# Optimization experiments

Measured on AMD Instinct MI355X. Metric: run time of the kernel, lower is better.

## Reference

```python
import jax, jax.numpy as jnp
import numpy as np

N = 4096      # nodes
INS = 256     # input feature dim
OUTS = 64     # per-mechanism output dim
M = 4         # N_mechs
LEAK = 0.2    # leaky relu negative slope
NEG_INF = -1e9


def setup_inputs() -> dict:
    key = jax.random.key(0)
    ks = jax.random.split(key, 7)
    x = jax.random.normal(ks[0], (N, INS), dtype=jnp.float32)
    adj = jax.random.randint(ks[1], (N, N), 0, 2).astype(jnp.int32)
    W = jax.random.normal(ks[2], (M, INS, OUTS), dtype=jnp.float32) * 0.1
    a1 = jax.random.normal(ks[3], (M, OUTS), dtype=jnp.float32) * 0.1
    a2 = jax.random.normal(ks[4], (M, OUTS), dtype=jnp.float32) * 0.1
    Wc = jax.random.normal(ks[5], (INS, 2 * M * OUTS), dtype=jnp.float32) * 0.1
    bc = jnp.zeros((2 * M * OUTS,), dtype=jnp.float32)
    return {"x": x, "adj": adj, "W": W, "a1": a1, "a2": a2, "Wc": Wc, "bc": bc}


def reference(x, adj, W, a1, a2, Wc, bc):
    # conditioner: mean-pool nodes -> linear -> (gamma, beta) per mechanism
    pooled = x.mean(axis=0)                                   # [INS]
    gb = (pooled @ Wc + bc).reshape(2, M, OUTS)
    gamma, beta = gb[0], gb[1]                                # [M, OUTS] each

    # per-mechanism linear transform + FiLM modulation
    h = jnp.einsum('ni,mio->mno', x, W)                       # [M, N, OUTS]
    h = gamma[:, None, :] * h + beta[:, None, :]

    # GAT-style decomposed attention logits: e_ij = leaky_relu(a1.h_i + a2.h_j)
    e_src = jnp.einsum('mno,mo->mn', h, a1)                   # [M, N]
    e_dst = jnp.einsum('mno,mo->mn', h, a2)                   # [M, N]
    e = e_src[:, :, None] + e_dst[:, None, :]                 # [M, N, N]
    e = jnp.where(e > 0, e, LEAK * e)                         # leaky relu

    # mask by adjacency, softmax over neighbors
    e = jnp.where(adj[None] > 0, e, jnp.float32(NEG_INF))
    attn = jax.nn.softmax(e, axis=-1)                         # [M, N, N]

    out = jnp.einsum('mnk,mko->mno', attn, h)                 # [M, N, OUTS]
    out = jnp.transpose(out, (1, 0, 2)).reshape(N, M * OUTS)  # concat dim=1
    return jax.nn.elu(out)                                    # activate=True
```

## Files before the change

### kernel.cpp

```cpp
#include <hip/hip_runtime.h>
#include <hip/hip_bf16.h>

#define NN    4096
#define INS_  256
#define OUTS_ 64
#define MM    4
#define LOG2E 1.4426950408889634f

typedef float f32x4 __attribute__((ext_vector_type(4)));
typedef short s16x8 __attribute__((ext_vector_type(8)));
typedef unsigned int u32x4 __attribute__((ext_vector_type(4)));

typedef const __attribute__((address_space(1))) unsigned char glob_u8;
typedef __attribute__((address_space(3))) unsigned char lds_u8;

__device__ __forceinline__ void stage16(const void* g, void* l) {
    __builtin_amdgcn_global_load_lds((glob_u8*)g, (lds_u8*)l, 16, 0, 0);
}

__device__ __forceinline__ unsigned int cvt_pk_bf16(float a, float b) {
    unsigned int r;
    asm("v_cvt_pk_bf16_f32 %0, %1, %2" : "=v"(r) : "v"(a), "v"(b));
    return r;
}

__device__ __forceinline__ unsigned int pack_bf16(float a, float b) {
    unsigned int ua = __builtin_bit_cast(unsigned int, a);
    unsigned int ub = __builtin_bit_cast(unsigned int, b);
    ua = (ua + 0x7FFFu + ((ua >> 16) & 1u)) >> 16;
    ub = (ub + 0x7FFFu + ((ub >> 16) & 1u)) & 0xFFFF0000u;
    return ua | ub;
}

__device__ __forceinline__ float mand(float w, unsigned mb, int e) {
    const int m = ((int)(mb << (31 - e))) >> 31;
    return __builtin_bit_cast(float, (__builtin_bit_cast(int, w) & m));
}

__device__ __forceinline__ s16x8 mk_af(float c, unsigned mb,
        const f32x4 q0, const f32x4 q1, const f32x4 q2, const f32x4 q3, float& z) {
    const float w0 = mand(fmaxf(q0[0], c * q0[1]), mb, 0);
    const float w1 = mand(fmaxf(q0[2], c * q0[3]), mb, 1);
    const float w2 = mand(fmaxf(q1[0], c * q1[1]), mb, 2);
    const float w3 = mand(fmaxf(q1[2], c * q1[3]), mb, 3);
    const float w4 = mand(fmaxf(q2[0], c * q2[1]), mb, 4);
    const float w5 = mand(fmaxf(q2[2], c * q2[3]), mb, 5);
    const float w6 = mand(fmaxf(q3[0], c * q3[1]), mb, 6);
    const float w7 = mand(fmaxf(q3[2], c * q3[3]), mb, 7);
    z += ((w0 + w1) + (w2 + w3)) + ((w4 + w5) + (w6 + w7));
    u32x4 au;
    au.x = cvt_pk_bf16(w0, w1);
    au.y = cvt_pk_bf16(w2, w3);
    au.z = cvt_pk_bf16(w4, w5);
    au.w = cvt_pk_bf16(w6, w7);
    return __builtin_bit_cast(s16x8, au);
}


__global__ __launch_bounds__(256) void k_prep(const int* __restrict__ adj,
                                              unsigned long long* __restrict__ msk,
                                              const float* __restrict__ x,
                                              float* __restrict__ part) {
    const int b = blockIdx.x;
    if (b < 1024) {
        const int lane = threadIdx.x & 63;
        const int w    = threadIdx.x >> 6;
        const int r    = b * 4 + w;
        const int* __restrict__ row = adj + (size_t)r * NN;
        unsigned long long* mrow = msk + (size_t)r * 64;
        #pragma unroll 1
        for (int c0 = 0; c0 < 64; c0 += 16) {
            int a[16];
            #pragma unroll
            for (int k = 0; k < 16; ++k) a[k] = row[(c0 + k) * 64 + lane];
            unsigned long long m[16];
            #pragma unroll
            for (int k = 0; k < 16; ++k) m[k] = __ballot(a[k] != 0);
            if (lane == 0) {
                #pragma unroll
                for (int k = 0; k < 16; ++k) mrow[c0 + k] = m[k];
            }
        }
    } else {
        const int bb = b - 1024;
        const int t  = threadIdx.x;
        const int r0 = bb * 64;
        float s = 0.f;
        #pragma unroll 8
        for (int r = 0; r < 64; ++r) s += x[(size_t)(r0 + r) * INS_ + t];
        part[bb * INS_ + t] = s;
    }
}

__global__ __launch_bounds__(256, 2) void k_filmc(
    const float* __restrict__ x, const float* __restrict__ W,
    const float* __restrict__ a1, const float* __restrict__ a2,
    const float* __restrict__ part, const float* __restrict__ Wc,
    const float* __restrict__ bc, float* __restrict__ sc,
    float* __restrict__ spq, unsigned char* __restrict__ htb)
{
    __shared__ float wlds[INS_ * OUTS_];
    __shared__ float sp[INS_];
    __shared__ float pg[256];
    __shared__ float gg[64], bbv[64];

    const int t  = threadIdx.x;
    const int o  = t & 63;
    const int wv = __builtin_amdgcn_readfirstlane(t >> 6);
    const int m  = blockIdx.y;
    const int n0 = blockIdx.x * 32 + wv * 8;

    {
        const unsigned char* wsrc = (const unsigned char*)W + (size_t)m * 65536 + t * 16;
        unsigned char* wdst = (unsigned char*)wlds + t * 16;
        #pragma unroll
        for (int it = 0; it < 16; ++it)
            stage16(wsrc + it * 4096, wdst + it * 4096);
    }

    {
        float s = 0.f;
        #pragma unroll 8
        for (int b = 0; b < 64; ++b) s += part[b * INS_ + t];
        sp[t] = s * (1.0f / NN);
    }
    __syncthreads();

    {
        const int half = t >> 7;
        const int idx  = t & 127;
        const int col  = m * 64 + (idx & 63) + ((idx & 64) ? 256 : 0);
        float acc = (half == 0) ? bc[col] : 0.f;
        const int ib = half * 128;
        #pragma unroll 8
        for (int i = 0; i < 128; ++i)
            acc = fmaf(sp[ib + i], Wc[(size_t)(ib + i) * 512 + col], acc);
        pg[t] = acc;
    }
    __syncthreads();
    if (t < 128) {
        const float v = pg[t] + pg[t + 128];
        if (t < 64) gg[t] = v; else bbv[t - 64] = v;
    }
    __syncthreads();

    float acc[8];
    #pragma unroll
    for (int k = 0; k < 8; ++k) acc[k] = 0.f;

    const float* xp = x + (size_t)n0 * INS_;

    #pragma unroll 4
    for (int i = 0; i < INS_; ++i) {
        const float wl = wlds[i * 64 + o];
        #pragma unroll
        for (int k = 0; k < 8; ++k)
            acc[k] = fmaf(xp[k * INS_ + i], wl, acc[k]);
    }

    const float ga  = gg[o];
    const float be  = bbv[o];
    const float va1 = a1[m * 64 + o];
    const float va2 = a2[m * 64 + o];

    float h[8], sv[8], dv[8];
    #pragma unroll
    for (int k = 0; k < 8; ++k) h[k] = fmaf(ga, acc[k], be);

    #pragma unroll
    for (int k = 0; k < 8; ++k) {
        float s1 = h[k] * va1;
        float s2 = h[k] * va2;
        #pragma unroll
        for (int off = 1; off < 64; off <<= 1) {
            s1 += __shfl_xor(s1, off);
            s2 += __shfl_xor(s2, off);
        }
        sv[k] = s1; dv[k] = s2;
    }

    u32x4 upk;
    upk.x = pack_bf16(h[0], h[1]);
    upk.y = pack_bf16(h[2], h[3]);
    upk.z = pack_bf16(h[4], h[5]);
    upk.w = pack_bf16(h[6], h[7]);
    const size_t phys = ((size_t)(m * 128 + blockIdx.x)) * 4096 + o * 64 + wv * 16;
    *reinterpret_cast<u32x4*>(htb + phys) = upk;

    const int lk = o & 7;
    float ssel = sv[0], dsel = dv[0];
    #pragma unroll
    for (int k = 1; k < 8; ++k) {
        if (lk == k) { ssel = sv[k]; dsel = dv[k]; }
    }
    if (o < 8) {
        sc[(size_t)m * NN + n0 + lk] = exp2f(-0.8f * LOG2E * ssel);
    } else if (o < 16) {
        const float spv = dsel * LOG2E;
        float2 ex = make_float2(exp2f(spv), exp2f(0.2f * spv));
        *reinterpret_cast<float2*>(&spq[(size_t)(m * NN + n0 + lk) * 2]) = ex;
    }
}

#define LOADT(tn, B) do {                                                  \
    const unsigned char* tb_ = tb0 + (size_t)(tn) * 4096;                  \
    B[0] = *reinterpret_cast<const s16x8*>(tb_);                           \
    B[1] = *reinterpret_cast<const s16x8*>(tb_ + 1024);                    \
    B[2] = *reinterpret_cast<const s16x8*>(tb_ + 2048);                    \
    B[3] = *reinterpret_cast<const s16x8*>(tb_ + 3072);                    \
} while (0)

#define COMPUTE(tn, B, mw0, mw1) do {                                      \
    const float* qp_ = pqb + (tn) * 64;                                    \
    const f32x4 q0_ = *reinterpret_cast<const f32x4*>(qp_);                \
    const f32x4 q1_ = *reinterpret_cast<const f32x4*>(qp_ + 4);            \
    const f32x4 q2_ = *reinterpret_cast<const f32x4*>(qp_ + 8);            \
    const f32x4 q3_ = *reinterpret_cast<const f32x4*>(qp_ + 12);           \
    const s16x8 Af0_ = mk_af(c0v, (mw0) >> sh, q0_, q1_, q2_, q3_, z0);    \
    const s16x8 Af1_ = mk_af(c1v, (mw1) >> sh, q0_, q1_, q2_, q3_, z1);    \
    acc0[0] = __builtin_amdgcn_mfma_f32_16x16x32_bf16(Af0_, B[0], acc0[0], 0, 0, 0); \
    acc0[1] = __builtin_amdgcn_mfma_f32_16x16x32_bf16(Af0_, B[1], acc0[1], 0, 0, 0); \
    acc0[2] = __builtin_amdgcn_mfma_f32_16x16x32_bf16(Af0_, B[2], acc0[2], 0, 0, 0); \
    acc0[3] = __builtin_amdgcn_mfma_f32_16x16x32_bf16(Af0_, B[3], acc0[3], 0, 0, 0); \
    acc1[0] = __builtin_amdgcn_mfma_f32_16x16x32_bf16(Af1_, B[0], acc1[0], 0, 0, 0); \
    acc1[1] = __builtin_amdgcn_mfma_f32_16x16x32_bf16(Af1_, B[1], acc1[1], 0, 0, 0); \
    acc1[2] = __builtin_amdgcn_mfma_f32_16x16x32_bf16(Af1_, B[2], acc1[2], 0, 0, 0); \
    acc1[3] = __builtin_amdgcn_mfma_f32_16x16x32_bf16(Af1_, B[3], acc1[3], 0, 0, 0); \
} while (0)

__global__ __launch_bounds__(512, 2) void k_attn(
    const unsigned int* __restrict__ msk, const float* __restrict__ sc,
    const float* __restrict__ spq, const unsigned char* __restrict__ htb,
    float* __restrict__ out)
{
    extern __shared__ float lds[];
    float* accP = lds;
    float* zP   = lds + 8 * 2048;

    const int t    = threadIdx.x;
    const int lane = t & 63;
    const int jq   = __builtin_amdgcn_readfirstlane(t >> 6);
    const int col  = lane & 15;
    const int kg   = lane >> 4;
    const int sh   = kg * 8;
    const int i0   = blockIdx.x * 32;
    const int mech = blockIdx.y;

    const float c0v = sc[(size_t)mech * NN + i0 + col];
    const float c1v = sc[(size_t)mech * NN + i0 + 16 + col];

    const u32x4* mr0 = reinterpret_cast<const u32x4*>(
        msk + (size_t)(i0 + col) * 128 + jq * 16);
    const u32x4* mr1 = reinterpret_cast<const u32x4*>(
        msk + (size_t)(i0 + 16 + col) * 128 + jq * 16);
    const float* pqb = spq + (size_t)mech * NN * 2 + (jq * 512 + kg * 8) * 2;
    const unsigned char* tb0 = htb + ((size_t)(mech * 128 + jq * 16)) * 4096
                             + col * 64 + kg * 16;

    f32x4 acc0[4], acc1[4];
    #pragma unroll
    for (int f = 0; f < 4; ++f) {
        acc0[f] = (f32x4){0.f, 0.f, 0.f, 0.f};
        acc1[f] = (f32x4){0.f, 0.f, 0.f, 0.f};
    }
    float z0 = 0.f, z1 = 0.f;

    s16x8 Ba[4], Bb[4];
    LOADT(0, Ba);
    u32x4 m0n = mr0[0];
    u32x4 m1n = mr1[0];

    #pragma unroll 1
    for (int tq = 0; tq < 4; ++tq) {
        const int base = tq * 4;
        const u32x4 m0 = m0n, m1 = m1n;
        if (tq < 3) { m0n = mr0[tq + 1]; m1n = mr1[tq + 1]; }
        LOADT(base + 1, Bb);
        COMPUTE(base + 0, Ba, m0[0], m1[0]);
        LOADT(base + 2, Ba);
        COMPUTE(base + 1, Bb, m0[1], m1[1]);
        LOADT(base + 3, Bb);
        COMPUTE(base + 2, Ba, m0[2], m1[2]);
        if (tq < 3) LOADT(base + 4, Ba);
        COMPUTE(base + 3, Bb, m0[3], m1[3]);
    }

    z0 += __shfl_xor(z0, 16); z0 += __shfl_xor(z0, 32);
    z1 += __shfl_xor(z1, 16); z1 += __shfl_xor(z1, 32);

    float* my = accP + jq * 2048;
    #pragma unroll
    for (int f = 0; f < 4; ++f) {
        #pragma unroll
        for (int rr = 0; rr < 4; ++rr) {
            my[(kg * 4 + rr) * 64 + f * 16 + col]      = acc0[f][rr];
            my[(16 + kg * 4 + rr) * 64 + f * 16 + col] = acc1[f][rr];
        }
    }
    if (lane < 16) {
        zP[jq * 32 + lane]      = z0;
        zP[jq * 32 + 16 + lane] = z1;
    }
    __syncthreads();

    const int row = t >> 4;
    const int o0  = (t & 15) * 4;
    f32x4 s = (f32x4){0.f, 0.f, 0.f, 0.f};
    float z = 0.f;
    #pragma unroll
    for (int p = 0; p < 8; ++p) {
        s += *reinterpret_cast<const f32x4*>(accP + p * 2048 + row * 64 + o0);
        z += zP[p * 32 + row];
    }
    const float inv = 1.0f / z;
    f32x4 res;
    #pragma unroll
    for (int e = 0; e < 4; ++e) {
        const float v = s[e] * inv;
        res[e] = v > 0.f ? v : expm1f(v);
    }
    *reinterpret_cast<f32x4*>(out + (size_t)(i0 + row) * 256 + mech * 64 + o0) = res;
}

extern "C" void kernel_launch(void* const* d_in, const int* in_sizes, int n_in,
                              void* d_out, int out_size, void* d_ws, size_t ws_size,
                              hipStream_t stream) {
    const float* x   = (const float*)d_in[0];
    const int*   adj = (const int*)d_in[1];
    const float* W   = (const float*)d_in[2];
    const float* a1  = (const float*)d_in[3];
    const float* a2  = (const float*)d_in[4];
    const float* Wc  = (const float*)d_in[5];
    const float* bc  = (const float*)d_in[6];
    float* out = (float*)d_out;

    float* wsf    = (float*)d_ws;
    float* part   = wsf;
    float* scv    = wsf + 16896;
    float* spq    = wsf + 33280;
    unsigned char* htb = (unsigned char*)(wsf + 66048);
    unsigned long long* msk = (unsigned long long*)(htb + (size_t)2097152);

    (void)hipFuncSetAttribute((const void*)k_attn,
                              hipFuncAttributeMaxDynamicSharedMemorySize, 66560);

    k_prep<<<1088, 256, 0, stream>>>(adj, msk, x, part);
    k_filmc<<<dim3(128, 4), 256, 0, stream>>>(x, W, a1, a2, part, Wc, bc, scv, spq, htb);
    k_attn<<<dim3(128, 4), 512, 66560, stream>>>((const unsigned int*)msk, scv, spq, htb, out);
}
```

Measured before the change: 81.03 us.

## Fuse adjacency bitmask packing into attention kernel and process all mechanisms per block

The adjacency-to-bitmask conversion moves out of the prep kernel and into the attention kernel. Each 1024-thread block now covers 16 rows for all four mechanisms and packs those rows' adjacency bits directly into LDS, so the global mask buffer is neither written nor read back. The pooling reduction becomes its own small kernel. In exchange each block does half as many rows per wave, there are longer key loops, and occupancy drops to one block per CU. The 64 MB adjacency read now sits on the attention kernel's critical path instead of in a separate launch.

```diff
diff --git a/kernel.cpp b/kernel.cpp
--- a/kernel.cpp
+++ b/kernel.cpp
@@ -57,39 +57,14 @@
 }
 
 
-__global__ __launch_bounds__(256) void k_prep(const int* __restrict__ adj,
-                                              unsigned long long* __restrict__ msk,
-                                              const float* __restrict__ x,
+__global__ __launch_bounds__(256) void k_pool(const float* __restrict__ x,
                                               float* __restrict__ part) {
-    const int b = blockIdx.x;
-    if (b < 1024) {
-        const int lane = threadIdx.x & 63;
-        const int w    = threadIdx.x >> 6;
-        const int r    = b * 4 + w;
-        const int* __restrict__ row = adj + (size_t)r * NN;
-        unsigned long long* mrow = msk + (size_t)r * 64;
-        #pragma unroll 1
-        for (int c0 = 0; c0 < 64; c0 += 16) {
-            int a[16];
-            #pragma unroll
-            for (int k = 0; k < 16; ++k) a[k] = row[(c0 + k) * 64 + lane];
-            unsigned long long m[16];
-            #pragma unroll
-            for (int k = 0; k < 16; ++k) m[k] = __ballot(a[k] != 0);
-            if (lane == 0) {
-                #pragma unroll
-                for (int k = 0; k < 16; ++k) mrow[c0 + k] = m[k];
-            }
-        }
-    } else {
-        const int bb = b - 1024;
-        const int t  = threadIdx.x;
-        const int r0 = bb * 64;
-        float s = 0.f;
-        #pragma unroll 8
-        for (int r = 0; r < 64; ++r) s += x[(size_t)(r0 + r) * INS_ + t];
-        part[bb * INS_ + t] = s;
-    }
+    const int t  = threadIdx.x;
+    const int r0 = blockIdx.x * 64;
+    float s = 0.f;
+    #pragma unroll 8
+    for (int r = 0; r < 64; ++r) s += x[(size_t)(r0 + r) * INS_ + t];
+    part[blockIdx.x * INS_ + t] = s;
 }
 
 __global__ __launch_bounds__(256, 2) void k_filmc(
@@ -202,6 +177,8 @@
     }
 }
 
+#define MROWW 132
+
 #define LOADT(tn, B) do {                                                  \
     const unsigned char* tb_ = tb0 + (size_t)(tn) * 4096;                  \
     B[0] = *reinterpret_cast<const s16x8*>(tb_);                           \
@@ -210,107 +187,111 @@
     B[3] = *reinterpret_cast<const s16x8*>(tb_ + 3072);                    \
 } while (0)
 
-#define COMPUTE(tn, B, mw0, mw1) do {                                      \
+#define COMPUTE1(tn, B, mw) do {                                           \
     const float* qp_ = pqb + (tn) * 64;                                    \
     const f32x4 q0_ = *reinterpret_cast<const f32x4*>(qp_);                \
     const f32x4 q1_ = *reinterpret_cast<const f32x4*>(qp_ + 4);            \
     const f32x4 q2_ = *reinterpret_cast<const f32x4*>(qp_ + 8);            \
     const f32x4 q3_ = *reinterpret_cast<const f32x4*>(qp_ + 12);           \
-    const s16x8 Af0_ = mk_af(c0v, (mw0) >> sh, q0_, q1_, q2_, q3_, z0);    \
-    const s16x8 Af1_ = mk_af(c1v, (mw1) >> sh, q0_, q1_, q2_, q3_, z1);    \
-    acc0[0] = __builtin_amdgcn_mfma_f32_16x16x32_bf16(Af0_, B[0], acc0[0], 0, 0, 0); \
-    acc0[1] = __builtin_amdgcn_mfma_f32_16x16x32_bf16(Af0_, B[1], acc0[1], 0, 0, 0); \
-    acc0[2] = __builtin_amdgcn_mfma_f32_16x16x32_bf16(Af0_, B[2], acc0[2], 0, 0, 0); \
-    acc0[3] = __builtin_amdgcn_mfma_f32_16x16x32_bf16(Af0_, B[3], acc0[3], 0, 0, 0); \
-    acc1[0] = __builtin_amdgcn_mfma_f32_16x16x32_bf16(Af1_, B[0], acc1[0], 0, 0, 0); \
-    acc1[1] = __builtin_amdgcn_mfma_f32_16x16x32_bf16(Af1_, B[1], acc1[1], 0, 0, 0); \
-    acc1[2] = __builtin_amdgcn_mfma_f32_16x16x32_bf16(Af1_, B[2], acc1[2], 0, 0, 0); \
-    acc1[3] = __builtin_amdgcn_mfma_f32_16x16x32_bf16(Af1_, B[3], acc1[3], 0, 0, 0); \
+    const s16x8 Af_ = mk_af(c0v, (mw) >> sh, q0_, q1_, q2_, q3_, z0);      \
+    acc[0] = __builtin_amdgcn_mfma_f32_16x16x32_bf16(Af_, B[0], acc[0], 0, 0, 0); \
+    acc[1] = __builtin_amdgcn_mfma_f32_16x16x32_bf16(Af_, B[1], acc[1], 0, 0, 0); \
+    acc[2] = __builtin_amdgcn_mfma_f32_16x16x32_bf16(Af_, B[2], acc[2], 0, 0, 0); \
+    acc[3] = __builtin_amdgcn_mfma_f32_16x16x32_bf16(Af_, B[3], acc[3], 0, 0, 0); \
 } while (0)
 
-__global__ __launch_bounds__(512, 2) void k_attn(
-    const unsigned int* __restrict__ msk, const float* __restrict__ sc,
+__global__ __launch_bounds__(1024, 1) void k_attn(
+    const int* __restrict__ adj, const float* __restrict__ sc,
     const float* __restrict__ spq, const unsigned char* __restrict__ htb,
     float* __restrict__ out)
 {
-    extern __shared__ float lds[];
-    float* accP = lds;
-    float* zP   = lds + 8 * 2048;
+    extern __shared__ unsigned char dlds[];
+    unsigned int* mlds = (unsigned int*)dlds;
+    float* accP = (float*)(dlds + 8448);
+    float* zP   = (float*)(dlds + 8448 + 65536);
 
     const int t    = threadIdx.x;
     const int lane = t & 63;
-    const int jq   = __builtin_amdgcn_readfirstlane(t >> 6);
+    const int w    = __builtin_amdgcn_readfirstlane(t >> 6);
+    const int mech = w & 3;
+    const int jq   = w >> 2;
     const int col  = lane & 15;
     const int kg   = lane >> 4;
     const int sh   = kg * 8;
-    const int i0   = blockIdx.x * 32;
-    const int mech = blockIdx.y;
+    const int i0   = blockIdx.x * 16;
+
+    {
+        const int* __restrict__ row = adj + (size_t)(i0 + w) * NN;
+        unsigned int* mrow = mlds + w * MROWW;
+        #pragma unroll 1
+        for (int c0 = 0; c0 < 64; c0 += 16) {
+            int a[16];
+            #pragma unroll
+            for (int k = 0; k < 16; ++k) a[k] = row[(c0 + k) * 64 + lane];
+            unsigned long long m[16];
+            #pragma unroll
+            for (int k = 0; k < 16; ++k) m[k] = __ballot(a[k] != 0);
+            if (lane == 0) {
+                #pragma unroll
+                for (int k = 0; k < 16; ++k)
+                    *reinterpret_cast<unsigned long long*>(mrow + (c0 + k) * 2) = m[k];
+            }
+        }
+    }
+    __syncthreads();
 
     const float c0v = sc[(size_t)mech * NN + i0 + col];
-    const float c1v = sc[(size_t)mech * NN + i0 + 16 + col];
-
-    const u32x4* mr0 = reinterpret_cast<const u32x4*>(
-        msk + (size_t)(i0 + col) * 128 + jq * 16);
-    const u32x4* mr1 = reinterpret_cast<const u32x4*>(
-        msk + (size_t)(i0 + 16 + col) * 128 + jq * 16);
-    const float* pqb = spq + (size_t)mech * NN * 2 + (jq * 512 + kg * 8) * 2;
-    const unsigned char* tb0 = htb + ((size_t)(mech * 128 + jq * 16)) * 4096
+    const u32x4* mr0 = reinterpret_cast<const u32x4*>(mlds + col * MROWW + jq * 32);
+    const float* pqb = spq + (size_t)mech * NN * 2 + (jq * 1024 + kg * 8) * 2;
+    const unsigned char* tb0 = htb + ((size_t)(mech * 128 + jq * 32)) * 4096
                              + col * 64 + kg * 16;
 
-    f32x4 acc0[4], acc1[4];
-    #pragma unroll
-    for (int f = 0; f < 4; ++f) {
-        acc0[f] = (f32x4){0.f, 0.f, 0.f, 0.f};
-        acc1[f] = (f32x4){0.f, 0.f, 0.f, 0.f};
-    }
-    float z0 = 0.f, z1 = 0.f;
+    f32x4 acc[4];
+    #pragma unroll
+    for (int f = 0; f < 4; ++f) acc[f] = (f32x4){0.f, 0.f, 0.f, 0.f};
+    float z0 = 0.f;
 
     s16x8 Ba[4], Bb[4];
     LOADT(0, Ba);
-    u32x4 m0n = mr0[0];
-    u32x4 m1n = mr1[0];
 
     #pragma unroll 1
-    for (int tq = 0; tq < 4; ++tq) {
+    for (int tq = 0; tq < 8; ++tq) {
         const int base = tq * 4;
-        const u32x4 m0 = m0n, m1 = m1n;
-        if (tq < 3) { m0n = mr0[tq + 1]; m1n = mr1[tq + 1]; }
+        const u32x4 m0 = mr0[tq];
         LOADT(base + 1, Bb);
-        COMPUTE(base + 0, Ba, m0[0], m1[0]);
+        COMPUTE1(base + 0, Ba, m0[0]);
         LOADT(base + 2, Ba);
-        COMPUTE(base + 1, Bb, m0[1], m1[1]);
+        COMPUTE1(base + 1, Bb, m0[1]);
         LOADT(base + 3, Bb);
-        COMPUTE(base + 2, Ba, m0[2], m1[2]);
-        if (tq < 3) LOADT(base + 4, Ba);
-        COMPUTE(base + 3, Bb, m0[3], m1[3]);
+        COMPUTE1(base + 2, Ba, m0[2]);
+        if (tq < 7) LOADT(base + 4, Ba);
+        COMPUTE1(base + 3, Bb, m0[3]);
     }
 
     z0 += __shfl_xor(z0, 16); z0 += __shfl_xor(z0, 32);
-    z1 += __shfl_xor(z1, 16); z1 += __shfl_xor(z1, 32);
-
-    float* my = accP + jq * 2048;
+
+    float* my = accP + w * 1024;
     #pragma unroll
     for (int f = 0; f < 4; ++f) {
         #pragma unroll
-        for (int rr = 0; rr < 4; ++rr) {
-            my[(kg * 4 + rr) * 64 + f * 16 + col]      = acc0[f][rr];
-            my[(16 + kg * 4 + rr) * 64 + f * 16 + col] = acc1[f][rr];
-        }
-    }
-    if (lane < 16) {
-        zP[jq * 32 + lane]      = z0;
-        zP[jq * 32 + 16 + lane] = z1;
-    }
-    __syncthreads();
-
-    const int row = t >> 4;
-    const int o0  = (t & 15) * 4;
+        for (int rr = 0; rr < 4; ++rr)
+            my[(kg * 4 + rr) * 64 + f * 16 + col] = acc[f][rr];
+    }
+    if (lane < 16) zP[w * 16 + lane] = z0;
+    __syncthreads();
+
+    const int f0    = t * 4;
+    const int row   = f0 >> 8;
+    const int mo    = f0 & 255;
+    const int mech2 = mo >> 6;
+    const int o0    = mo & 63;
     f32x4 s = (f32x4){0.f, 0.f, 0.f, 0.f};
     float z = 0.f;
     #pragma unroll
-    for (int p = 0; p < 8; ++p) {
-        s += *reinterpret_cast<const f32x4*>(accP + p * 2048 + row * 64 + o0);
-        z += zP[p * 32 + row];
+    for (int p = 0; p < 4; ++p) {
+        const int wp = p * 4 + mech2;
+        s += *reinterpret_cast<const f32x4*>(accP + wp * 1024 + row * 64 + o0);
+        z += zP[wp * 16 + row];
     }
     const float inv = 1.0f / z;
     f32x4 res;
@@ -319,7 +300,7 @@
         const float v = s[e] * inv;
         res[e] = v > 0.f ? v : expm1f(v);
     }
-    *reinterpret_cast<f32x4*>(out + (size_t)(i0 + row) * 256 + mech * 64 + o0) = res;
+    *reinterpret_cast<f32x4*>(out + (size_t)(i0 + row) * 256 + mo) = res;
 }
 
 extern "C" void kernel_launch(void* const* d_in, const int* in_sizes, int n_in,
@@ -339,12 +320,11 @@
     float* scv    = wsf + 16896;
     float* spq    = wsf + 33280;
     unsigned char* htb = (unsigned char*)(wsf + 66048);
-    unsigned long long* msk = (unsigned long long*)(htb + (size_t)2097152);
 
     (void)hipFuncSetAttribute((const void*)k_attn,
-                              hipFuncAttributeMaxDynamicSharedMemorySize, 66560);
-
-    k_prep<<<1088, 256, 0, stream>>>(adj, msk, x, part);
+                              hipFuncAttributeMaxDynamicSharedMemorySize, 75008);
+
+    k_pool<<<64, 256, 0, stream>>>(x, part);
     k_filmc<<<dim3(128, 4), 256, 0, stream>>>(x, W, a1, a2, part, Wc, bc, scv, spq, htb);
-    k_attn<<<dim3(128, 4), 512, 66560, stream>>>((const unsigned int*)msk, scv, spq, htb, out);
-}
+    k_attn<<<256, 1024, 75008, stream>>>(adj, scv, spq, htb, out);
+}
```

Result: slower. 98.29 us (+21.3%).
